# Optimization experiments

Hardware: AMD Instinct MI355X
Metric: run time of the kernel (lower is better)

The kernel has to match this reference:

```python
import jax, jax.numpy as jnp
import numpy as np

B, L, H, E, R = 2, 512, 768, 512, 32768
H2 = H // 2


def setup_inputs() -> dict:
    key = jax.random.key(0)
    ks = jax.random.split(key, 16)
    s = 0.02
    inp = {
        "hidden_states": jax.random.normal(ks[0], (B, L, H), dtype=jnp.float32),
        "ent_start": jax.random.randint(ks[1], (B, E), 0, L, dtype=jnp.int32),
        "ent_label": jax.random.randint(ks[2], (B, E), 0, 3, dtype=jnp.int32),
        "rel_head": jax.random.randint(ks[3], (B, R), 0, E, dtype=jnp.int32),
        "rel_tail": jax.random.randint(ks[4], (B, R), 0, E, dtype=jnp.int32),
        "rel_label": jax.random.randint(ks[5], (B, R), 0, 2, dtype=jnp.int32),
        "entity_emb": jax.random.normal(ks[6], (3, H), dtype=jnp.float32) * s,
        "head_W1": jax.random.normal(ks[7], (2 * H, H), dtype=jnp.float32) * s,
        "head_b1": jnp.zeros((H,), dtype=jnp.float32),
        "head_W2": jax.random.normal(ks[8], (H, H2), dtype=jnp.float32) * s,
        "head_b2": jnp.zeros((H2,), dtype=jnp.float32),
        "tail_W1": jax.random.normal(ks[9], (2 * H, H), dtype=jnp.float32) * s,
        "tail_b1": jnp.zeros((H,), dtype=jnp.float32),
        "tail_W2": jax.random.normal(ks[10], (H, H2), dtype=jnp.float32) * s,
        "tail_b2": jnp.zeros((H2,), dtype=jnp.float32),
        "bil_W": jax.random.normal(ks[11], (2, H2, H2), dtype=jnp.float32) * s,
        "lin_W": jax.random.normal(ks[12], (2 * H2, 2), dtype=jnp.float32) * s,
        "lin_b": jnp.zeros((2,), dtype=jnp.float32),
    }
    return inp


def _mlp(x, W1, b1, W2, b2):
    # Linear -> ReLU -> (dropout=identity) -> Linear -> ReLU -> (dropout=identity)
    h = jax.nn.relu(jnp.einsum("brd,dh->brh", x, W1) + b1)
    return jax.nn.relu(jnp.einsum("brh,hk->brk", h, W2) + b2)


def reference(hidden_states, ent_start, ent_label, rel_head, rel_tail, rel_label,
              entity_emb, head_W1, head_b1, head_W2, head_b2,
              tail_W1, tail_b1, tail_W2, tail_b2, bil_W, lin_W, lin_b):
    # Gather entity start token index and label for each relation endpoint
    h_idx = jnp.take_along_axis(ent_start, rel_head, axis=1)  # [B,R]
    t_idx = jnp.take_along_axis(ent_start, rel_tail, axis=1)
    h_lab = jnp.take_along_axis(ent_label, rel_head, axis=1)
    t_lab = jnp.take_along_axis(ent_label, rel_tail, axis=1)

    # Gather hidden states at entity start positions: [B,R,H]
    h_tok = jnp.take_along_axis(hidden_states, h_idx[..., None], axis=1)
    t_tok = jnp.take_along_axis(hidden_states, t_idx[..., None], axis=1)

    head_repr = jnp.concatenate([h_tok, entity_emb[h_lab]], axis=-1)  # [B,R,2H]
    tail_repr = jnp.concatenate([t_tok, entity_emb[t_lab]], axis=-1)

    heads = _mlp(head_repr, head_W1, head_b1, head_W2, head_b2)  # [B,R,H2]
    tails = _mlp(tail_repr, tail_W1, tail_b1, tail_W2, tail_b2)

    # BiaffineAttention: bilinear(x1,x2) + linear(cat(x1,x2))
    bil = jnp.einsum("brd,ode,bre->bro", heads, bil_W, tails)  # [B,R,2]
    lin = jnp.einsum("brc,co->bro", jnp.concatenate([heads, tails], axis=-1), lin_W) + lin_b
    logits = bil + lin  # [B,R,2]

    # Per-doc mean cross-entropy, summed over docs (matches loss accumulation)
    logp = jax.nn.log_softmax(logits, axis=-1)
    ce = -jnp.take_along_axis(logp, rel_label[..., None], axis=-1)[..., 0]  # [B,R]
    loss = ce.mean(axis=-1).sum()

    return loss, logits.reshape(B * R, 2)
```

## Files before the change

kernel.cpp:

```cpp
#include <hip/hip_runtime.h>
#include <math.h>

#define BB 2
#define LL 512
#define HH 768
#define EE 512
#define RR 32768
#define H2 384
#define MM 1024

typedef __attribute__((ext_vector_type(8))) short     bf16x8;
typedef __attribute__((ext_vector_type(4))) float     f32x4;
typedef __attribute__((ext_vector_type(8))) unsigned short u16x8;

__device__ __forceinline__ unsigned short f2bf(float f) {
    unsigned int u = __float_as_uint(f);
    u = (u + 0x7FFFu + ((u >> 16) & 1u)) >> 16;
    return (unsigned short)u;
}

__global__ __launch_bounds__(256) void prep(
    const float* __restrict__ hW1, const float* __restrict__ tW1,
    const float* __restrict__ hW2, const float* __restrict__ tW2,
    const float* __restrict__ bilW,
    unsigned short* __restrict__ W1ht, unsigned short* __restrict__ W1tt,
    unsigned short* __restrict__ W2ht, unsigned short* __restrict__ W2tt,
    unsigned short* __restrict__ bW0t, unsigned short* __restrict__ bW1t,
    const float* __restrict__ hidden, const int* __restrict__ ent_start,
    const int* __restrict__ ent_label, const float* __restrict__ emb,
    unsigned short* __restrict__ Xbf)
{
    __shared__ unsigned short T[32 * 40];
    const int bid = blockIdx.x;
    const int t = threadIdx.x;

    if (bid >= 3168) {
        const int m = bid - 3168;
        if (t >= 192) return;
        const int b = m >> 9;
        const int idx = ent_start[m];
        const int lab = ent_label[m];
        float4 v0, v1;
        if (t < 96) {
            const float4* s = (const float4*)(hidden + (size_t)(b * LL + idx) * HH);
            v0 = s[2 * t]; v1 = s[2 * t + 1];
        } else {
            const float4* s = (const float4*)(emb + (size_t)lab * HH);
            v0 = s[2 * t - 192]; v1 = s[2 * t - 191];
        }
        u16x8 o;
        o[0] = f2bf(v0.x); o[1] = f2bf(v0.y); o[2] = f2bf(v0.z); o[3] = f2bf(v0.w);
        o[4] = f2bf(v1.x); o[5] = f2bf(v1.y); o[6] = f2bf(v1.z); o[7] = f2bf(v1.w);
        *(u16x8*)(Xbf + (size_t)m * 1536 + 8 * t) = o;
        return;
    }

    const float* src; unsigned short* dst; int K, N, tile;
    if (bid < 1152)      { src = hW1;            dst = W1ht; K = 1536; N = 768; tile = bid; }
    else if (bid < 2304) { src = tW1;            dst = W1tt; K = 1536; N = 768; tile = bid - 1152; }
    else if (bid < 2592) { src = hW2;            dst = W2ht; K = 768;  N = 384; tile = bid - 2304; }
    else if (bid < 2880) { src = tW2;            dst = W2tt; K = 768;  N = 384; tile = bid - 2592; }
    else if (bid < 3024) { src = bilW;           dst = bW0t; K = 384;  N = 384; tile = bid - 2880; }
    else                 { src = bilW + 384*384; dst = bW1t; K = 384;  N = 384; tile = bid - 3024; }
    const int tn = N >> 5;
    const int n0 = (tile % tn) * 32;
    const int k0 = (tile / tn) * 32;

    const int r  = t >> 3;
    const int c4 = (t & 7) * 4;
    const float4 g = *(const float4*)(src + (size_t)(k0 + r) * N + n0 + c4);
    T[(c4 + 0) * 40 + r] = f2bf(g.x);
    T[(c4 + 1) * 40 + r] = f2bf(g.y);
    T[(c4 + 2) * 40 + r] = f2bf(g.z);
    T[(c4 + 3) * 40 + r] = f2bf(g.w);
    __syncthreads();
    const int n  = t >> 3;
    const int k4 = (t & 7) * 4;
    *(ushort4*)(dst + (size_t)(n0 + n) * K + k0 + k4) = *(ushort4*)&T[n * 40 + k4];
}

template<bool RELU, bool BIAS, bool WF32, bool WBF16>
__global__ __launch_bounds__(256) void gemm_mfma(
    const unsigned short* __restrict__ A, int lda, int aoff1,
    const unsigned short* __restrict__ Bt0, const unsigned short* __restrict__ Bt1,
    int ldb, int bt_mrow, int Nh,
    const float* __restrict__ bias0, const float* __restrict__ bias1,
    int K, float* __restrict__ Cf, unsigned short* __restrict__ Cb, int ldc)
{
    __shared__ unsigned short As[64 * 40];
    __shared__ unsigned short Bs[64 * 40];

    const int tid = threadIdx.x;
    const int n0 = blockIdx.x * 64;
    const int m0 = blockIdx.y * 64;
    const int hf = (n0 >= Nh) ? 1 : 0;
    const unsigned short* Bt = hf ? Bt1 : Bt0;
    const int nc0 = n0 - (hf ? Nh : 0);
    const int aoff = hf ? aoff1 : 0;

    const int sr = tid >> 2;
    const int sk = (tid & 3) * 8;

    const unsigned short* Ap = A + (size_t)(m0 + sr) * lda + aoff + sk;
    const unsigned short* Bp = Bt + (size_t)((m0 >> 9) * bt_mrow + nc0 + sr) * ldb + sk;

    const int lane = tid & 63;
    const int wave = tid >> 6;
    const int wm = (wave & 1) * 32;
    const int wn = (wave >> 1) * 32;
    const int l15 = lane & 15;
    const int quad = lane >> 4;

    f32x4 acc00 = {}, acc01 = {}, acc10 = {}, acc11 = {};

    for (int k0 = 0; k0 < K; k0 += 32) {
        const u16x8 av = *(const u16x8*)(Ap + k0);
        const u16x8 bv = *(const u16x8*)(Bp + k0);
        __syncthreads();
        *(u16x8*)&As[sr * 40 + sk] = av;
        *(u16x8*)&Bs[sr * 40 + sk] = bv;
        __syncthreads();
        const bf16x8 a0 = *(const bf16x8*)&As[(wm + l15) * 40 + quad * 8];
        const bf16x8 a1 = *(const bf16x8*)&As[(wm + 16 + l15) * 40 + quad * 8];
        const bf16x8 b0 = *(const bf16x8*)&Bs[(wn + l15) * 40 + quad * 8];
        const bf16x8 b1 = *(const bf16x8*)&Bs[(wn + 16 + l15) * 40 + quad * 8];
        acc00 = __builtin_amdgcn_mfma_f32_16x16x32_bf16(a0, b0, acc00, 0, 0, 0);
        acc01 = __builtin_amdgcn_mfma_f32_16x16x32_bf16(a0, b1, acc01, 0, 0, 0);
        acc10 = __builtin_amdgcn_mfma_f32_16x16x32_bf16(a1, b0, acc10, 0, 0, 0);
        acc11 = __builtin_amdgcn_mfma_f32_16x16x32_bf16(a1, b1, acc11, 0, 0, 0);
    }

    float bias_v0 = 0.f, bias_v1 = 0.f;
    if (BIAS) {
        const float* bb = hf ? bias1 : bias0;
        bias_v0 = bb[nc0 + wn + l15];
        bias_v1 = bb[nc0 + wn + 16 + l15];
    }
    const f32x4 accs[2][2] = {{acc00, acc01}, {acc10, acc11}};
    #pragma unroll
    for (int mi = 0; mi < 2; ++mi) {
        #pragma unroll
        for (int ni = 0; ni < 2; ++ni) {
            const int col = n0 + wn + ni * 16 + l15;
            const float bv = ni ? bias_v1 : bias_v0;
            #pragma unroll
            for (int r = 0; r < 4; ++r) {
                const int row = m0 + wm + mi * 16 + quad * 4 + r;
                float v = accs[mi][ni][r];
                if (BIAS) v += bv;
                if (RELU) v = fmaxf(v, 0.f);
                if (WF32) Cf[(size_t)row * ldc + col] = v;
                if (WBF16) Cb[(size_t)row * ldc + col] = f2bf(v);
            }
        }
    }
}

__global__ __launch_bounds__(256) void lin_proj(
    const float* __restrict__ HT, const float* __restrict__ linW,
    float* __restrict__ hlin, float* __restrict__ tlin)
{
    const int tid = threadIdx.x;
    const int lane = tid & 63;
    const int wave = tid >> 6;
    const int m = blockIdx.x * 4 + wave;
    const float* hr = HT + (size_t)m * 768;
    const float* tr = hr + 384;
    float hl0 = 0.f, hl1 = 0.f, tl0 = 0.f, tl1 = 0.f;
    #pragma unroll
    for (int t = 0; t < 6; ++t) {
        const int c = lane + 64 * t;
        const float hv = hr[c];
        const float tv = tr[c];
        const float2 wh = *(const float2*)(linW + 2 * c);
        const float2 wt = *(const float2*)(linW + 2 * (384 + c));
        hl0 += hv * wh.x; hl1 += hv * wh.y;
        tl0 += tv * wt.x; tl1 += tv * wt.y;
    }
    #pragma unroll
    for (int o = 32; o >= 1; o >>= 1) {
        hl0 += __shfl_xor(hl0, o, 64);
        hl1 += __shfl_xor(hl1, o, 64);
        tl0 += __shfl_xor(tl0, o, 64);
        tl1 += __shfl_xor(tl1, o, 64);
    }
    if (lane == 0) {
        hlin[2 * m]     = hl0;
        hlin[2 * m + 1] = hl1;
        tlin[2 * m]     = tl0;
        tlin[2 * m + 1] = tl1;
    }
}

__global__ __launch_bounds__(256) void rel_gather(
    const float* __restrict__ Stab,
    const float* __restrict__ hlin, const float* __restrict__ tlin,
    const float* __restrict__ lin_b,
    const int* __restrict__ rel_head, const int* __restrict__ rel_tail,
    const int* __restrict__ rel_label,
    float* __restrict__ out, float* __restrict__ bsum)
{
    const int tid = threadIdx.x;
    const int i = blockIdx.x * 256 + tid;
    const int b = i >> 15;
    const int h = rel_head[i];
    const int t = rel_tail[i];
    const int lab = rel_label[i];
    const int mh = (b << 9) + h;
    const int mt = (b << 9) + t;

    const float2 hl = ((const float2*)hlin)[mh];
    const float2 tl = ((const float2*)tlin)[mt];
    const float* srow = Stab + (size_t)mh * 1024;
    const float z0 = srow[t]       + hl.x + tl.x + lin_b[0];
    const float z1 = srow[512 + t] + hl.y + tl.y + lin_b[1];
    out[1 + 2 * (size_t)i]     = z0;
    out[2 + 2 * (size_t)i]     = z1;

    const float mx = fmaxf(z0, z1);
    const float mn = fminf(z0, z1);
    const float lse = mx + log1pf(expf(mn - mx));
    float ce = lse - (lab ? z1 : z0);

    #pragma unroll
    for (int o = 32; o >= 1; o >>= 1) ce += __shfl_xor(ce, o, 64);
    __shared__ float wsum[4];
    if ((tid & 63) == 0) wsum[tid >> 6] = ce;
    __syncthreads();
    if (tid == 0) bsum[blockIdx.x] = wsum[0] + wsum[1] + wsum[2] + wsum[3];
}

__global__ __launch_bounds__(256) void finalize(
    const float* __restrict__ bsum, float* __restrict__ out)
{
    const int tid = threadIdx.x;
    float v = bsum[tid];
    #pragma unroll
    for (int o = 32; o >= 1; o >>= 1) v += __shfl_xor(v, o, 64);
    __shared__ float s[4];
    if ((tid & 63) == 0) s[tid >> 6] = v;
    __syncthreads();
    if (tid == 0) {
        out[0] = (s[0] + s[1] + s[2] + s[3]) * (1.0f / (float)RR);
    }
}

extern "C" void kernel_launch(void* const* d_in, const int* in_sizes, int n_in,
                              void* d_out, int out_size, void* d_ws, size_t ws_size,
                              hipStream_t stream) {
    const float* hidden    = (const float*)d_in[0];
    const int*   ent_start = (const int*)d_in[1];
    const int*   ent_label = (const int*)d_in[2];
    const int*   rel_head  = (const int*)d_in[3];
    const int*   rel_tail  = (const int*)d_in[4];
    const int*   rel_label = (const int*)d_in[5];
    const float* emb       = (const float*)d_in[6];
    const float* head_W1   = (const float*)d_in[7];
    const float* head_b1   = (const float*)d_in[8];
    const float* head_W2   = (const float*)d_in[9];
    const float* head_b2   = (const float*)d_in[10];
    const float* tail_W1   = (const float*)d_in[11];
    const float* tail_b1   = (const float*)d_in[12];
    const float* tail_W2   = (const float*)d_in[13];
    const float* tail_b2   = (const float*)d_in[14];
    const float* bil_W     = (const float*)d_in[15];
    const float* lin_W     = (const float*)d_in[16];
    const float* lin_b     = (const float*)d_in[17];
    float* out = (float*)d_out;

    char* w = (char*)d_ws;
    auto carve = [&](size_t bytes) {
        char* p = w; w += (bytes + 255) & ~(size_t)255; return p;
    };
    unsigned short* Xbf  = (unsigned short*)carve((size_t)MM * 1536 * 2);
    unsigned short* Y1bf = (unsigned short*)carve((size_t)MM * 1536 * 2);
    unsigned short* HTbf = (unsigned short*)carve((size_t)MM * 768 * 2);
    float*          HT   = (float*)carve((size_t)MM * 768 * 4);
    unsigned short* hWbf = (unsigned short*)carve((size_t)MM * 768 * 2);
    float*          Stab = (float*)carve((size_t)MM * 1024 * 4);
    unsigned short* W1ht = (unsigned short*)carve((size_t)768 * 1536 * 2);
    unsigned short* W1tt = (unsigned short*)carve((size_t)768 * 1536 * 2);
    unsigned short* W2ht = (unsigned short*)carve((size_t)384 * 768 * 2);
    unsigned short* W2tt = (unsigned short*)carve((size_t)384 * 768 * 2);
    unsigned short* bW0t = (unsigned short*)carve((size_t)384 * 384 * 2);
    unsigned short* bW1t = (unsigned short*)carve((size_t)384 * 384 * 2);
    float*          hlin = (float*)carve(2048 * 4);
    float*          tlin = (float*)carve(2048 * 4);
    float*          bsum = (float*)carve(256 * 4);

    prep<<<4192, 256, 0, stream>>>(
        head_W1, tail_W1, head_W2, tail_W2, bil_W,
        W1ht, W1tt, W2ht, W2tt, bW0t, bW1t,
        hidden, ent_start, ent_label, emb, Xbf);

    gemm_mfma<true, true, false, true><<<dim3(24, 16), 256, 0, stream>>>(
        Xbf, 1536, 0, W1ht, W1tt, 1536, 0, 768, head_b1, tail_b1, 1536,
        nullptr, Y1bf, 1536);

    gemm_mfma<true, true, true, true><<<dim3(12, 16), 256, 0, stream>>>(
        Y1bf, 1536, 768, W2ht, W2tt, 768, 0, 384, head_b2, tail_b2, 768,
        HT, HTbf, 768);

    gemm_mfma<false, false, false, true><<<dim3(12, 16), 256, 0, stream>>>(
        HTbf, 768, 0, bW0t, bW1t, 384, 0, 384, nullptr, nullptr, 384,
        nullptr, hWbf, 768);

    gemm_mfma<false, false, true, false><<<dim3(16, 16), 256, 0, stream>>>(
        hWbf, 768, 384, HTbf + 384, HTbf + 384, 768, 512, 512,
        nullptr, nullptr, 384, Stab, nullptr, 1024);

    lin_proj<<<256, 256, 0, stream>>>(HT, lin_W, hlin, tlin);

    rel_gather<<<256, 256, 0, stream>>>(Stab, hlin, tlin, lin_b,
                                        rel_head, rel_tail, rel_label, out, bsum);

    finalize<<<1, 256, 0, stream>>>(bsum, out);
}
```

Baseline: 161.4 us.

## Fuse linear projection into GEMM epilogues and finalize into rel_gather

The linear-term projection moves into the second-layer GEMM epilogue, which accumulates it with shuffles and atomics. The bias and linear terms are folded into the score-table GEMM epilogue, and the separate lin_proj and finalize kernels are removed. The loss is reduced with an atomic accumulator plus a last-block counter. This saves two launches and the fp32 HT write and read, at the cost of atomics and a zero-init step in prep that must finish before the GEMMs run.

```diff
diff --git a/kernel.cpp b/kernel.cpp
--- a/kernel.cpp
+++ b/kernel.cpp
@@ -28,11 +28,17 @@
     unsigned short* __restrict__ bW0t, unsigned short* __restrict__ bW1t,
     const float* __restrict__ hidden, const int* __restrict__ ent_start,
     const int* __restrict__ ent_label, const float* __restrict__ emb,
-    unsigned short* __restrict__ Xbf)
+    unsigned short* __restrict__ Xbf, float* __restrict__ small)
 {
     __shared__ unsigned short T[32 * 40];
     const int bid = blockIdx.x;
     const int t = threadIdx.x;
+
+    if (bid == 0) {
+        #pragma unroll
+        for (int i = t; i < 4096; i += 256) small[i] = 0.f;
+        if (t == 0) { small[4096] = 0.f; ((int*)small)[4097] = 0; }
+    }
 
     if (bid >= 3168) {
         const int m = bid - 3168;
@@ -79,13 +85,16 @@
     *(ushort4*)(dst + (size_t)(n0 + n) * K + k0 + k4) = *(ushort4*)&T[n * 40 + k4];
 }
 
-template<bool RELU, bool BIAS, bool WF32, bool WBF16>
+template<bool RELU, bool BIAS, bool WF32, bool WBF16, bool LINACC, bool LINADD>
 __global__ __launch_bounds__(256) void gemm_mfma(
     const unsigned short* __restrict__ A, int lda, int aoff1,
     const unsigned short* __restrict__ Bt0, const unsigned short* __restrict__ Bt1,
     int ldb, int bt_mrow, int Nh,
     const float* __restrict__ bias0, const float* __restrict__ bias1,
-    int K, float* __restrict__ Cf, unsigned short* __restrict__ Cb, int ldc)
+    int K, float* __restrict__ Cf, unsigned short* __restrict__ Cb, int ldc,
+    const float* __restrict__ linW, float* __restrict__ hlinA, float* __restrict__ tlinA,
+    const float* __restrict__ hlinR, const float* __restrict__ tlinR,
+    const float* __restrict__ lin_b)
 {
     __shared__ unsigned short As[64 * 40];
     __shared__ unsigned short Bs[64 * 40];
@@ -130,75 +139,72 @@
         acc11 = __builtin_amdgcn_mfma_f32_16x16x32_bf16(a1, b1, acc11, 0, 0, 0);
     }
 
-    float bias_v0 = 0.f, bias_v1 = 0.f;
+    float bias_v[2] = {0.f, 0.f};
     if (BIAS) {
         const float* bb = hf ? bias1 : bias0;
-        bias_v0 = bb[nc0 + wn + l15];
-        bias_v1 = bb[nc0 + wn + 16 + l15];
-    }
+        bias_v[0] = bb[nc0 + wn + l15];
+        bias_v[1] = bb[nc0 + wn + 16 + l15];
+    }
+    float wl0[2], wl1[2];
+    if (LINACC) {
+        #pragma unroll
+        for (int ni = 0; ni < 2; ++ni) {
+            const int nc = nc0 + wn + ni * 16 + l15;
+            const float* wp = linW + 2 * (hf * 384 + nc);
+            wl0[ni] = wp[0]; wl1[ni] = wp[1];
+        }
+    }
+    float la0[2][4] = {}, la1[2][4] = {};
+
     const f32x4 accs[2][2] = {{acc00, acc01}, {acc10, acc11}};
     #pragma unroll
     for (int mi = 0; mi < 2; ++mi) {
         #pragma unroll
         for (int ni = 0; ni < 2; ++ni) {
             const int col = n0 + wn + ni * 16 + l15;
-            const float bv = ni ? bias_v1 : bias_v0;
             #pragma unroll
             for (int r = 0; r < 4; ++r) {
                 const int row = m0 + wm + mi * 16 + quad * 4 + r;
                 float v = accs[mi][ni][r];
-                if (BIAS) v += bv;
+                if (BIAS) v += bias_v[ni];
                 if (RELU) v = fmaxf(v, 0.f);
+                if (LINACC) { la0[mi][r] += v * wl0[ni]; la1[mi][r] += v * wl1[ni]; }
+                if (LINADD) {
+                    const int mt = (m0 >> 9) * bt_mrow + (nc0 + wn + ni * 16 + l15);
+                    v += hlinR[2 * row + hf] + tlinR[2 * mt + hf] + lin_b[hf];
+                }
                 if (WF32) Cf[(size_t)row * ldc + col] = v;
                 if (WBF16) Cb[(size_t)row * ldc + col] = f2bf(v);
             }
         }
     }
-}
-
-__global__ __launch_bounds__(256) void lin_proj(
-    const float* __restrict__ HT, const float* __restrict__ linW,
-    float* __restrict__ hlin, float* __restrict__ tlin)
-{
-    const int tid = threadIdx.x;
-    const int lane = tid & 63;
-    const int wave = tid >> 6;
-    const int m = blockIdx.x * 4 + wave;
-    const float* hr = HT + (size_t)m * 768;
-    const float* tr = hr + 384;
-    float hl0 = 0.f, hl1 = 0.f, tl0 = 0.f, tl1 = 0.f;
-    #pragma unroll
-    for (int t = 0; t < 6; ++t) {
-        const int c = lane + 64 * t;
-        const float hv = hr[c];
-        const float tv = tr[c];
-        const float2 wh = *(const float2*)(linW + 2 * c);
-        const float2 wt = *(const float2*)(linW + 2 * (384 + c));
-        hl0 += hv * wh.x; hl1 += hv * wh.y;
-        tl0 += tv * wt.x; tl1 += tv * wt.y;
-    }
-    #pragma unroll
-    for (int o = 32; o >= 1; o >>= 1) {
-        hl0 += __shfl_xor(hl0, o, 64);
-        hl1 += __shfl_xor(hl1, o, 64);
-        tl0 += __shfl_xor(tl0, o, 64);
-        tl1 += __shfl_xor(tl1, o, 64);
-    }
-    if (lane == 0) {
-        hlin[2 * m]     = hl0;
-        hlin[2 * m + 1] = hl1;
-        tlin[2 * m]     = tl0;
-        tlin[2 * m + 1] = tl1;
+
+    if (LINACC) {
+        #pragma unroll
+        for (int mi = 0; mi < 2; ++mi)
+            #pragma unroll
+            for (int r = 0; r < 4; ++r) {
+                float s0 = la0[mi][r], s1 = la1[mi][r];
+                #pragma unroll
+                for (int o = 8; o >= 1; o >>= 1) {
+                    s0 += __shfl_xor(s0, o, 64);
+                    s1 += __shfl_xor(s1, o, 64);
+                }
+                if (l15 == 0) {
+                    const int row = m0 + wm + mi * 16 + quad * 4 + r;
+                    float* dst = (hf ? tlinA : hlinA) + 2 * row;
+                    atomicAdd(dst, s0);
+                    atomicAdd(dst + 1, s1);
+                }
+            }
     }
 }
 
 __global__ __launch_bounds__(256) void rel_gather(
     const float* __restrict__ Stab,
-    const float* __restrict__ hlin, const float* __restrict__ tlin,
-    const float* __restrict__ lin_b,
     const int* __restrict__ rel_head, const int* __restrict__ rel_tail,
     const int* __restrict__ rel_label,
-    float* __restrict__ out, float* __restrict__ bsum)
+    float* __restrict__ out, float* __restrict__ loss_acc, int* __restrict__ counter)
 {
     const int tid = threadIdx.x;
     const int i = blockIdx.x * 256 + tid;
@@ -207,15 +213,12 @@
     const int t = rel_tail[i];
     const int lab = rel_label[i];
     const int mh = (b << 9) + h;
-    const int mt = (b << 9) + t;
-
-    const float2 hl = ((const float2*)hlin)[mh];
-    const float2 tl = ((const float2*)tlin)[mt];
+
     const float* srow = Stab + (size_t)mh * 1024;
-    const float z0 = srow[t]       + hl.x + tl.x + lin_b[0];
-    const float z1 = srow[512 + t] + hl.y + tl.y + lin_b[1];
-    out[1 + 2 * (size_t)i]     = z0;
-    out[2 + 2 * (size_t)i]     = z1;
+    const float z0 = srow[t];
+    const float z1 = srow[512 + t];
+    out[1 + 2 * (size_t)i] = z0;
+    out[2 + 2 * (size_t)i] = z1;
 
     const float mx = fmaxf(z0, z1);
     const float mn = fminf(z0, z1);
@@ -227,21 +230,15 @@
     __shared__ float wsum[4];
     if ((tid & 63) == 0) wsum[tid >> 6] = ce;
     __syncthreads();
-    if (tid == 0) bsum[blockIdx.x] = wsum[0] + wsum[1] + wsum[2] + wsum[3];
-}
-
-__global__ __launch_bounds__(256) void finalize(
-    const float* __restrict__ bsum, float* __restrict__ out)
-{
-    const int tid = threadIdx.x;
-    float v = bsum[tid];
-    #pragma unroll
-    for (int o = 32; o >= 1; o >>= 1) v += __shfl_xor(v, o, 64);
-    __shared__ float s[4];
-    if ((tid & 63) == 0) s[tid >> 6] = v;
-    __syncthreads();
     if (tid == 0) {
-        out[0] = (s[0] + s[1] + s[2] + s[3]) * (1.0f / (float)RR);
+        const float s = wsum[0] + wsum[1] + wsum[2] + wsum[3];
+        atomicAdd(loss_acc, s);
+        __threadfence();
+        const int old = atomicAdd(counter, 1);
+        if (old == (int)gridDim.x - 1) {
+            const float tot = atomicAdd(loss_acc, 0.0f);
+            out[0] = tot * (1.0f / (float)RR);
+        }
     }
 }
 
@@ -275,7 +272,6 @@
     unsigned short* Xbf  = (unsigned short*)carve((size_t)MM * 1536 * 2);
     unsigned short* Y1bf = (unsigned short*)carve((size_t)MM * 1536 * 2);
     unsigned short* HTbf = (unsigned short*)carve((size_t)MM * 768 * 2);
-    float*          HT   = (float*)carve((size_t)MM * 768 * 4);
     unsigned short* hWbf = (unsigned short*)carve((size_t)MM * 768 * 2);
     float*          Stab = (float*)carve((size_t)MM * 1024 * 4);
     unsigned short* W1ht = (unsigned short*)carve((size_t)768 * 1536 * 2);
@@ -284,35 +280,34 @@
     unsigned short* W2tt = (unsigned short*)carve((size_t)384 * 768 * 2);
     unsigned short* bW0t = (unsigned short*)carve((size_t)384 * 384 * 2);
     unsigned short* bW1t = (unsigned short*)carve((size_t)384 * 384 * 2);
-    float*          hlin = (float*)carve(2048 * 4);
-    float*          tlin = (float*)carve(2048 * 4);
-    float*          bsum = (float*)carve(256 * 4);
+    float*          small = (float*)carve(4112 * 4);
+    float*          hlin  = small;
+    float*          tlin  = small + 2048;
+    float*          loss_acc = small + 4096;
+    int*            counter  = (int*)(small + 4097);
 
     prep<<<4192, 256, 0, stream>>>(
         head_W1, tail_W1, head_W2, tail_W2, bil_W,
         W1ht, W1tt, W2ht, W2tt, bW0t, bW1t,
-        hidden, ent_start, ent_label, emb, Xbf);
-
-    gemm_mfma<true, true, false, true><<<dim3(24, 16), 256, 0, stream>>>(
+        hidden, ent_start, ent_label, emb, Xbf, small);
+
+    gemm_mfma<true, true, false, true, false, false><<<dim3(24, 16), 256, 0, stream>>>(
         Xbf, 1536, 0, W1ht, W1tt, 1536, 0, 768, head_b1, tail_b1, 1536,
-        nullptr, Y1bf, 1536);
-
-    gemm_mfma<true, true, true, true><<<dim3(12, 16), 256, 0, stream>>>(
+        nullptr, Y1bf, 1536, nullptr, nullptr, nullptr, nullptr, nullptr, nullptr);
+
+    gemm_mfma<true, true, false, true, true, false><<<dim3(12, 16), 256, 0, stream>>>(
         Y1bf, 1536, 768, W2ht, W2tt, 768, 0, 384, head_b2, tail_b2, 768,
-        HT, HTbf, 768);
-
-    gemm_mfma<false, false, false, true><<<dim3(12, 16), 256, 0, stream>>>(
+        nullptr, HTbf, 768, lin_W, hlin, tlin, nullptr, nullptr, nullptr);
+
+    gemm_mfma<false, false, false, true, false, false><<<dim3(12, 16), 256, 0, stream>>>(
         HTbf, 768, 0, bW0t, bW1t, 384, 0, 384, nullptr, nullptr, 384,
-        nullptr, hWbf, 768);
-
-    gemm_mfma<false, false, true, false><<<dim3(16, 16), 256, 0, stream>>>(
+        nullptr, hWbf, 768, nullptr, nullptr, nullptr, nullptr, nullptr, nullptr);
+
+    gemm_mfma<false, false, true, false, false, true><<<dim3(16, 16), 256, 0, stream>>>(
         hWbf, 768, 384, HTbf + 384, HTbf + 384, 768, 512, 512,
-        nullptr, nullptr, 384, Stab, nullptr, 1024);
-
-    lin_proj<<<256, 256, 0, stream>>>(HT, lin_W, hlin, tlin);
-
-    rel_gather<<<256, 256, 0, stream>>>(Stab, hlin, tlin, lin_b,
-                                        rel_head, rel_tail, rel_label, out, bsum);
-
-    finalize<<<1, 256, 0, stream>>>(bsum, out);
-}
+        nullptr, nullptr, 384, Stab, nullptr, 1024,
+        nullptr, nullptr, nullptr, hlin, tlin, lin_b);
+
+    rel_gather<<<256, 256, 0, stream>>>(Stab, rel_head, rel_tail, rel_label,
+                                        out, loss_acc, counter);
+}
```

Result: slower. 165.4 us (+2.5%).
